# Performance work log

Measured on AMD Instinct MI355X. Metric: run time of the kernel, lower is better.

The kernel has to match this reference:

```python
import jax, jax.numpy as jnp
import numpy as np

DIM, NH, WS, SS, MLP_RATIO = 192, 6, 8, 4, 4
EPS = 1e-5


def _rel_pos_index(ws):
    coords = np.stack(np.meshgrid(np.arange(ws), np.arange(ws), indexing='ij')).reshape(2, -1)
    rel = (coords[:, :, None] - coords[:, None, :]).transpose(1, 2, 0)
    rel[:, :, 0] += ws - 1
    rel[:, :, 1] += ws - 1
    rel[:, :, 0] *= 2 * ws - 1
    return rel.sum(-1)  # (ws*ws, ws*ws) int


def _attn_mask(hp, wp, ws, ss):
    img = np.zeros((hp, wp))
    slices = (slice(0, -ws), slice(-ws, -ss), slice(-ss, None))
    cnt = 0
    for hs in slices:
        for vs in slices:
            img[hs, vs] = cnt
            cnt += 1
    mw = img.reshape(hp // ws, ws, wp // ws, ws).transpose(0, 2, 1, 3).reshape(-1, ws * ws)
    am = mw[:, None, :] - mw[:, :, None]  # (nW, N, N)
    return jnp.asarray(np.where(am != 0, -100.0, 0.0).astype(np.float32))


def _ln(x, g, b):
    mu = jnp.mean(x, axis=-1, keepdims=True)
    var = jnp.mean(jnp.square(x - mu), axis=-1, keepdims=True)
    return (x - mu) * jax.lax.rsqrt(var + EPS) * g + b


def setup_inputs():
    key = jax.random.key(0)
    ks = jax.random.split(key, 8)
    B, H, W, C = 8, 128, 128, DIM
    hid = C * MLP_RATIO
    n = lambda k, s: jax.random.normal(k, s, dtype=jnp.float32) * 0.02
    return {
        'x': jax.random.normal(ks[0], (B, H * W, C), dtype=jnp.float32),
        'h': H, 'w': W,
        'norm1_g': jnp.ones((C,), jnp.float32), 'norm1_b': jnp.zeros((C,), jnp.float32),
        'qkv_w': n(ks[1], (C, 3 * C)), 'qkv_b': jnp.zeros((3 * C,), jnp.float32),
        'proj_w': n(ks[2], (C, C)), 'proj_b': jnp.zeros((C,), jnp.float32),
        'rel_bias_table': n(ks[3], ((2 * WS - 1) ** 2, NH)),
        'norm2_g': jnp.ones((C,), jnp.float32), 'norm2_b': jnp.zeros((C,), jnp.float32),
        'fc1_w': n(ks[4], (C, hid)), 'fc1_b': jnp.zeros((hid,), jnp.float32),
        'fc2_w': n(ks[5], (hid, C)), 'fc2_b': jnp.zeros((C,), jnp.float32),
    }


def reference(x, h, w, norm1_g, norm1_b, qkv_w, qkv_b, proj_w, proj_b,
              rel_bias_table, norm2_g, norm2_b, fc1_w, fc1_b, fc2_w, fc2_b):
    B, L, C = x.shape
    ws, ss, nh = WS, SS, NH
    hd = C // nh
    scale = hd ** (-0.5)

    shortcut = x
    xg = _ln(x, norm1_g, norm1_b).reshape(B, h, w, C)

    pad_h = (-h) % ws
    pad_w = (-w) % ws
    if pad_h or pad_w:
        xg = jnp.pad(xg, ((0, 0), (0, pad_h), (0, pad_w), (0, 0)))
    hp, wp = h + pad_h, w + pad_w
    if ss > 0:
        xg = jnp.roll(xg, (-ss, -ss), axis=(1, 2))

    # window partition -> (nB, N, C)
    win = xg.reshape(B, hp // ws, ws, wp // ws, ws, C).transpose(0, 1, 3, 2, 4, 5).reshape(-1, ws * ws, C)
    nB, N, _ = win.shape

    qkv = (win @ qkv_w + qkv_b).reshape(nB, N, 3, nh, hd).transpose(2, 0, 3, 1, 4)
    q, k, v = qkv[0] * scale, qkv[1], qkv[2]  # (nB, nh, N, hd)

    attn = jnp.einsum('bhnd,bhmd->bhnm', q, k)  # (nB, nh, N, N)
    rpi = _rel_pos_index(ws)
    bias = rel_bias_table[rpi.reshape(-1)].reshape(N, N, nh).transpose(2, 0, 1)
    attn = attn + bias[None]
    if ss > 0:
        mask = _attn_mask(hp, wp, ws, ss)  # (nW, N, N)
        nW = mask.shape[0]
        attn = (attn.reshape(nB // nW, nW, nh, N, N) + mask[None, :, None]).reshape(nB, nh, N, N)
    attn = jax.nn.softmax(attn, axis=-1)

    out = jnp.einsum('bhnm,bhmd->bnhd', attn, v).reshape(nB, N, C)
    out = out @ proj_w + proj_b

    # window reverse
    out = out.reshape(B, hp // ws, wp // ws, ws, ws, C).transpose(0, 1, 3, 2, 4, 5).reshape(B, hp, wp, C)
    if ss > 0:
        out = jnp.roll(out, (ss, ss), axis=(1, 2))
    out = out[:, :h, :w].reshape(B, h * w, C)

    x = shortcut + out
    xn2 = _ln(x, norm2_g, norm2_b)
    mlp = jax.nn.gelu(xn2 @ fc1_w + fc1_b, approximate=False) @ fc2_w + fc2_b
    return x + mlp
```

## Files before the change

kernel.cpp:

```cpp
#include <hip/hip_runtime.h>

typedef unsigned short u16;
typedef unsigned int   u32;
typedef __attribute__((ext_vector_type(8))) short bf16x8;
typedef __attribute__((ext_vector_type(4))) float f32x4;

#define L_TOK   16384
#define C_DIM   192
#define HID_DIM 768

#define OFF_QKV  0
#define OFF_PROJ 110592
#define OFF_FC1  147456
#define OFF_FC2  294912
#define CVT_TOT  442368

union FragU { int4 i4; bf16x8 h8; };

#define MFMA_B16(a,b,c) __builtin_amdgcn_mfma_f32_16x16x32_bf16(a,b,c,0,0,0)

__device__ __forceinline__ u16 f2bf(float f) {
    u32 t; __builtin_memcpy(&t, &f, 4);
    t += 0x7FFFu + ((t >> 16) & 1u);
    return (u16)(t >> 16);
}

__global__ __launch_bounds__(256) void k_cvt(
    const float* __restrict__ qkvw, const float* __restrict__ projw,
    const float* __restrict__ fc1w, const float* __restrict__ fc2w,
    u16* __restrict__ ws)
{
    const int i = blockIdx.x * 256 + threadIdx.x;
    if (i >= CVT_TOT) return;
    float v; int dst;
    if (i < OFF_PROJ) {
        const int k = i / 576, col = i % 576;
        const int grp = col / 192, rem = col % 192;
        const int head = rem >> 5, dim = rem & 31;
        v = qkvw[i];
        dst = OFF_QKV + head * (96 * 192) + (grp * 32 + dim) * 192 + k;
    } else if (i < OFF_FC1) {
        const int s = i - OFF_PROJ;
        const int cin = s / 192, cout = s % 192;
        const int head = cin >> 5, j = cin & 31;
        v = projw[s];
        dst = OFF_PROJ + head * (192 * 32) + cout * 32 + j;
    } else if (i < OFF_FC2) {
        const int s = i - OFF_FC1;
        const int k = s / 768, h = s % 768;
        v = fc1w[s];
        dst = OFF_FC1 + h * 192 + k;
    } else {
        const int s = i - OFF_FC2;
        const int h = s / 192, c = s % 192;
        v = fc2w[s];
        dst = OFF_FC2 + c * 768 + h;
    }
    ws[dst] = f2bf(v);
}

__global__ __launch_bounds__(256, 2) void k_attnproj(
    const float* __restrict__ x, const float* __restrict__ g1v, const float* __restrict__ b1v,
    const u16* __restrict__ qkvwT, const float* __restrict__ qkvb,
    const float* __restrict__ relb, const u16* __restrict__ projT, const float* __restrict__ projb,
    float* __restrict__ x1)
{
    struct PW {
        u16 qsb[64 * 40];
        u16 ksb[64 * 40];
        u16 vsbT[32 * 72];
        u16 psb[64 * 72];
        u16 oh [64 * 40];
    };
    union SmemU {
        u16 xw[128 * 200];
        PW pw[2];
    };
    __shared__ __align__(16) SmemU u;
    __shared__ __align__(16) u16 wbuf[192 * 40];
    __shared__ float relbs[225 * 6];

    const int t  = threadIdx.x;
    const int lane = t & 63, w = t >> 6;
    const int win = w >> 1, half = w & 1;
    const int l15 = lane & 15, quad = lane >> 4;
    const int wi2 = blockIdx.x * 2 + win;
    const int b  = wi2 >> 8;
    const int hb = (wi2 >> 4) & 15;
    const int wb = wi2 & 15;
    const bool maskon = (hb == 15) || (wb == 15);
    const f32x4 zf = {0.f, 0.f, 0.f, 0.f};

    for (int i = t; i < 225 * 6; i += 256) relbs[i] = relb[i];

    #pragma unroll
    for (int tk = 0; tk < 2; ++tk) {
        const int nn = t >> 2, q4 = t & 3;
        const int tok = tk * 64 + nn;
        const int tw = tok >> 6, n = tok & 63;
        const int wiA = blockIdx.x * 2 + tw;
        const int bA  = wiA >> 8;
        const int hbA = (wiA >> 4) & 15, wbA = wiA & 15;
        const int r = n >> 3, c = n & 7;
        const int ho = (hbA * 8 + r + 4) & 127;
        const int wo = (wbA * 8 + c + 4) & 127;
        const size_t xoff = ((size_t)bA * L_TOK + ho * 128 + wo) * C_DIM;
        const float* xp = x + xoff + q4 * 48;
        float f[48];
        float sum = 0.f, sq = 0.f;
        #pragma unroll
        for (int i = 0; i < 12; ++i) {
            float4 v = *(const float4*)(xp + i * 4);
            f[i*4+0]=v.x; f[i*4+1]=v.y; f[i*4+2]=v.z; f[i*4+3]=v.w;
            sum += v.x+v.y+v.z+v.w;
            sq  += v.x*v.x + v.y*v.y + v.z*v.z + v.w*v.w;
        }
        sum += __shfl_xor(sum, 1); sum += __shfl_xor(sum, 2);
        sq  += __shfl_xor(sq, 1);  sq  += __shfl_xor(sq, 2);
        const float mu = sum * (1.f / 192.f);
        const float rstd = rsqrtf(sq * (1.f / 192.f) - mu * mu + 1e-5f);
        u16* xrow = u.xw + tok * 200 + q4 * 48;
        #pragma unroll
        for (int i = 0; i < 6; ++i) {
            u32 pk[4];
            #pragma unroll
            for (int j = 0; j < 4; ++j) {
                float g0 = g1v[q4*48 + i*8 + j*2],     b0 = b1v[q4*48 + i*8 + j*2];
                float g1 = g1v[q4*48 + i*8 + j*2 + 1], b1 = b1v[q4*48 + i*8 + j*2 + 1];
                float y0 = (f[i*8+j*2]   - mu) * rstd * g0 + b0;
                float y1 = (f[i*8+j*2+1] - mu) * rstd * g1 + b1;
                pk[j] = (u32)f2bf(y0) | (((u32)f2bf(y1)) << 16);
            }
            *(int4*)(xrow + i * 8) = make_int4((int)pk[0], (int)pk[1], (int)pk[2], (int)pk[3]);
        }
    }
    __syncthreads();

    FragU afrag[2][6];
    #pragma unroll
    for (int mt = 0; mt < 2; ++mt)
        #pragma unroll
        for (int kk = 0; kk < 6; ++kk)
            afrag[mt][kk].i4 = *(const int4*)(u.xw +
                (win*64 + half*32 + mt*16 + l15) * 200 + kk*32 + quad*8);

    PW* P = &u.pw[win];
    const int rb = half*32 + quad*4;

    int4 wr0, wr1, wr2;
    auto LOADW = [&](int hh, int sub) {
        if (sub < 3) {
            const u16* src = qkvwT + (size_t)hh * (96 * 192) + sub * 64;
            wr0 = *(const int4*)(src + ((t      ) >> 3) * 192 + ((t      ) & 7) * 8);
            wr1 = *(const int4*)(src + ((t + 256) >> 3) * 192 + ((t + 256) & 7) * 8);
            wr2 = *(const int4*)(src + ((t + 512) >> 3) * 192 + ((t + 512) & 7) * 8);
        } else {
            const u16* src = projT + (size_t)hh * (192 * 32);
            wr0 = *(const int4*)(src + ((t      ) >> 2) * 32 + ((t      ) & 3) * 8);
            wr1 = *(const int4*)(src + ((t + 256) >> 2) * 32 + ((t + 256) & 3) * 8);
            wr2 = *(const int4*)(src + ((t + 512) >> 2) * 32 + ((t + 512) & 3) * 8);
        }
    };
    auto STOREW = [&](int sub) {
        if (sub < 3) {
            *(int4*)(wbuf + ((t      ) >> 3) * 72 + ((t      ) & 7) * 8) = wr0;
            *(int4*)(wbuf + ((t + 256) >> 3) * 72 + ((t + 256) & 7) * 8) = wr1;
            *(int4*)(wbuf + ((t + 512) >> 3) * 72 + ((t + 512) & 7) * 8) = wr2;
        } else {
            *(int4*)(wbuf + ((t      ) >> 2) * 40 + ((t      ) & 3) * 8) = wr0;
            *(int4*)(wbuf + ((t + 256) >> 2) * 40 + ((t + 256) & 3) * 8) = wr1;
            *(int4*)(wbuf + ((t + 512) >> 2) * 40 + ((t + 512) & 3) * 8) = wr2;
        }
    };
    LOADW(0, 0);

    f32x4 acc2[2][12];
    #pragma unroll
    for (int mt = 0; mt < 2; ++mt)
        #pragma unroll
        for (int nt = 0; nt < 12; ++nt) acc2[mt][nt] = zf;

    for (int head = 0; head < 6; ++head) {
        f32x4 accq[2][6];
        #pragma unroll
        for (int mt = 0; mt < 2; ++mt)
            #pragma unroll
            for (int nt = 0; nt < 6; ++nt) accq[mt][nt] = zf;

        for (int kc = 0; kc < 3; ++kc) {
            __syncthreads();
            STOREW(kc);
            __syncthreads();
            LOADW(head, kc + 1);
            #pragma unroll
            for (int s = 0; s < 2; ++s) {
                #pragma unroll
                for (int nt = 0; nt < 6; ++nt) {
                    FragU bf_;
                    bf_.i4 = *(const int4*)(wbuf + (nt*16 + l15)*72 + s*32 + quad*8);
                    accq[0][nt] = MFMA_B16(afrag[0][kc*2 + s].h8, bf_.h8, accq[0][nt]);
                    accq[1][nt] = MFMA_B16(afrag[1][kc*2 + s].h8, bf_.h8, accq[1][nt]);
                }
            }
        }
        #pragma unroll
        for (int mt = 0; mt < 2; ++mt) {
            #pragma unroll
            for (int nt = 0; nt < 6; ++nt) {
                const int grp = nt >> 1;
                const int dim = (nt & 1)*16 + l15;
                const float bias = qkvb[grp*192 + head*32 + dim];
                float vv[4];
                #pragma unroll
                for (int rg = 0; rg < 4; ++rg) vv[rg] = accq[mt][nt][rg] + bias;
                const int rowb = rb + mt*16;
                if (grp == 0) {
                    #pragma unroll
                    for (int rg = 0; rg < 4; ++rg)
                        P->qsb[(rowb + rg)*40 + dim] = f2bf(vv[rg] * 0.17677669529663687f);
                } else if (grp == 1) {
                    #pragma unroll
                    for (int rg = 0; rg < 4; ++rg)
                        P->ksb[(rowb + rg)*40 + dim] = f2bf(vv[rg]);
                } else {
                    u32 lo = (u32)f2bf(vv[0]) | (((u32)f2bf(vv[1])) << 16);
                    u32 hi = (u32)f2bf(vv[2]) | (((u32)f2bf(vv[3])) << 16);
                    *(uint2*)&P->vsbT[dim*72 + rowb] = make_uint2(lo, hi);
                }
            }
        }
        __syncthreads();

        FragU qf0, qf1;
        qf0.i4 = *(const int4*)(P->qsb + (half*32 + l15)*40 + quad*8);
        qf1.i4 = *(const int4*)(P->qsb + (half*32 + 16 + l15)*40 + quad*8);
        f32x4 sv[2][4];
        #pragma unroll
        for (int nt = 0; nt < 4; ++nt) {
            FragU kf; kf.i4 = *(const int4*)(P->ksb + (nt*16 + l15)*40 + quad*8);
            sv[0][nt] = MFMA_B16(qf0.h8, kf.h8, zf);
            sv[1][nt] = MFMA_B16(qf1.h8, kf.h8, zf);
        }
        const int kr_ = l15 >> 3, kc2 = l15 & 7;
        #pragma unroll
        for (int mt = 0; mt < 2; ++mt) {
            #pragma unroll
            for (int rg = 0; rg < 4; ++rg) {
                const int qm = rb + mt*16 + rg;
                const int qr = qm >> 3, qc = qm & 7;
                #pragma unroll
                for (int nt = 0; nt < 4; ++nt) {
                    const int kr = nt*2 + kr_;
                    sv[mt][nt][rg] += relbs[((qr - kr + 7)*15 + (qc - kc2 + 7))*6 + head];
                }
            }
        }
        if (maskon) {
            #pragma unroll
            for (int mt = 0; mt < 2; ++mt) {
                #pragma unroll
                for (int rg = 0; rg < 4; ++rg) {
                    const int qm = rb + mt*16 + rg;
                    const int qr = qm >> 3, qc = qm & 7;
                    const int regq = ((hb == 15) ? (qr < 4 ? 1 : 2) : 0) * 3
                                   + ((wb == 15) ? (qc < 4 ? 1 : 2) : 0);
                    #pragma unroll
                    for (int nt = 0; nt < 4; ++nt) {
                        const int kr = nt*2 + kr_;
                        const int regk = ((hb == 15) ? (kr < 4 ? 1 : 2) : 0) * 3
                                       + ((wb == 15) ? (kc2 < 4 ? 1 : 2) : 0);
                        if (regq != regk) sv[mt][nt][rg] -= 100.f;
                    }
                }
            }
        }
        #pragma unroll
        for (int mt = 0; mt < 2; ++mt) {
            #pragma unroll
            for (int rg = 0; rg < 4; ++rg) {
                float mx = fmaxf(fmaxf(sv[mt][0][rg], sv[mt][1][rg]),
                                 fmaxf(sv[mt][2][rg], sv[mt][3][rg]));
                mx = fmaxf(mx, __shfl_xor(mx, 1));
                mx = fmaxf(mx, __shfl_xor(mx, 2));
                mx = fmaxf(mx, __shfl_xor(mx, 4));
                mx = fmaxf(mx, __shfl_xor(mx, 8));
                float s0 = 0.f;
                #pragma unroll
                for (int nt = 0; nt < 4; ++nt) {
                    sv[mt][nt][rg] = __expf(sv[mt][nt][rg] - mx); s0 += sv[mt][nt][rg];
                }
                s0 += __shfl_xor(s0, 1); s0 += __shfl_xor(s0, 2);
                s0 += __shfl_xor(s0, 4); s0 += __shfl_xor(s0, 8);
                const float inv = 1.f / s0;
                #pragma unroll
                for (int nt = 0; nt < 4; ++nt)
                    P->psb[(rb + mt*16 + rg)*72 + nt*16 + l15] = f2bf(sv[mt][nt][rg] * inv);
            }
        }

        FragU vb[2][2];
        #pragma unroll
        for (int ntv = 0; ntv < 2; ++ntv) {
            vb[ntv][0].i4 = *(const int4*)(P->vsbT + (ntv*16 + l15)*72 + quad*8);
            vb[ntv][1].i4 = *(const int4*)(P->vsbT + (ntv*16 + l15)*72 + 32 + quad*8);
        }
        #pragma unroll
        for (int mt = 0; mt < 2; ++mt) {
            FragU pa0, pa1;
            pa0.i4 = *(const int4*)(P->psb + (half*32 + mt*16 + l15)*72 + quad*8);
            pa1.i4 = *(const int4*)(P->psb + (half*32 + mt*16 + l15)*72 + 32 + quad*8);
            f32x4 ov0 = zf, ov1 = zf;
            ov0 = MFMA_B16(pa0.h8, vb[0][0].h8, ov0);
            ov0 = MFMA_B16(pa1.h8, vb[0][1].h8, ov0);
            ov1 = MFMA_B16(pa0.h8, vb[1][0].h8, ov1);
            ov1 = MFMA_B16(pa1.h8, vb[1][1].h8, ov1);
            #pragma unroll
            for (int rg = 0; rg < 4; ++rg) {
                P->oh[(rb + mt*16 + rg)*40 + l15]      = f2bf(ov0[rg]);
                P->oh[(rb + mt*16 + rg)*40 + 16 + l15] = f2bf(ov1[rg]);
            }
        }

        STOREW(3);
        __syncthreads();
        if (head < 5) LOADW(head + 1, 0);
        FragU ao0, ao1;
        ao0.i4 = *(const int4*)(P->oh + (half*32 + l15)*40 + quad*8);
        ao1.i4 = *(const int4*)(P->oh + (half*32 + 16 + l15)*40 + quad*8);
        #pragma unroll
        for (int nt = 0; nt < 12; ++nt) {
            FragU bp; bp.i4 = *(const int4*)(wbuf + (nt*16 + l15)*40 + quad*8);
            acc2[0][nt] = MFMA_B16(ao0.h8, bp.h8, acc2[0][nt]);
            acc2[1][nt] = MFMA_B16(ao1.h8, bp.h8, acc2[1][nt]);
        }
    }

    {
        float pb[12];
        #pragma unroll
        for (int nt = 0; nt < 12; ++nt) pb[nt] = projb[nt*16 + l15];
        #pragma unroll
        for (int mt = 0; mt < 2; ++mt) {
            #pragma unroll
            for (int rg = 0; rg < 4; ++rg) {
                const int tok = rb + mt*16 + rg;
                const int tr = tok >> 3, tc = tok & 7;
                const int ho2 = (hb * 8 + tr + 4) & 127;
                const int wo2 = (wb * 8 + tc + 4) & 127;
                const size_t base = ((size_t)b * L_TOK + ho2 * 128 + wo2) * C_DIM;
                #pragma unroll
                for (int nt = 0; nt < 12; ++nt) {
                    const int col = nt*16 + l15;
                    x1[base + col] = acc2[mt][nt][rg] + pb[nt] + x[base + col];
                }
            }
        }
    }
}

__global__ __launch_bounds__(256, 2) void k_mlp(
    const float* x1, const float* __restrict__ g2v, const float* __restrict__ b2v,
    const u16* __restrict__ fc1wT, const float* __restrict__ fc1b,
    const u16* __restrict__ fc2wT, const float* __restrict__ fc2b,
    float* out)
{
    union SmemU {
        u16 xnA[64 * 200];
        u16 hbuf[128 * 104];
    };
    __shared__ __align__(16) SmemU u;
    __shared__ __align__(16) u16 wT[2][7680];

    const int blk = blockIdx.x;
    const int t = threadIdx.x;
    const size_t row0 = (size_t)blk * 128;
    const int lane = t & 63, w = t >> 6;
    const int l15 = lane & 15, quad = lane >> 4;
    const f32x4 zf = {0.f, 0.f, 0.f, 0.f};

    FragU afrag[2][6];
    for (int hf = 0; hf < 2; ++hf) {
        const int nn = t >> 2, q4 = t & 3;
        const int tok = hf * 64 + nn;
        const float* xp = x1 + (row0 + tok) * C_DIM + q4 * 48;
        float f[48];
        float sum = 0.f, sq = 0.f;
        #pragma unroll
        for (int i = 0; i < 12; ++i) {
            float4 v = *(const float4*)(xp + i * 4);
            f[i*4+0]=v.x; f[i*4+1]=v.y; f[i*4+2]=v.z; f[i*4+3]=v.w;
            sum += v.x+v.y+v.z+v.w;
            sq  += v.x*v.x + v.y*v.y + v.z*v.z + v.w*v.w;
        }
        sum += __shfl_xor(sum,1); sum += __shfl_xor(sum,2);
        sq  += __shfl_xor(sq,1);  sq  += __shfl_xor(sq,2);
        const float mu = sum * (1.f/192.f);
        const float rstd = rsqrtf(sq * (1.f/192.f) - mu*mu + 1e-5f);
        u16* xrow = u.xnA + nn * 200 + q4 * 48;
        #pragma unroll
        for (int i = 0; i < 6; ++i) {
            u32 pk[4];
            #pragma unroll
            for (int j = 0; j < 4; ++j) {
                float g0 = g2v[q4*48 + i*8 + j*2],     b0 = b2v[q4*48 + i*8 + j*2];
                float g1 = g2v[q4*48 + i*8 + j*2 + 1], b1 = b2v[q4*48 + i*8 + j*2 + 1];
                float y0 = (f[i*8+j*2]   - mu) * rstd * g0 + b0;
                float y1 = (f[i*8+j*2+1] - mu) * rstd * g1 + b1;
                pk[j] = (u32)f2bf(y0) | (((u32)f2bf(y1)) << 16);
            }
            *(int4*)(xrow + i*8) = make_int4((int)pk[0], (int)pk[1], (int)pk[2], (int)pk[3]);
        }
        __syncthreads();
        #pragma unroll
        for (int kk = 0; kk < 6; ++kk)
            afrag[hf][kk].i4 = *(const int4*)(u.xnA + (w*16 + l15) * 200 + kk*32 + quad*8);
        __syncthreads();
    }

    int4 wr0, wr1, wr2;
    auto LOADW = [&](int hcL, int sub) {
        if (sub < 3) {
            const u16* src = fc1wT + (size_t)(hcL * 96) * 192 + sub * 64;
            wr0 = *(const int4*)(src + ((t      ) >> 3) * 192 + ((t      ) & 7) * 8);
            wr1 = *(const int4*)(src + ((t + 256) >> 3) * 192 + ((t + 256) & 7) * 8);
            wr2 = *(const int4*)(src + ((t + 512) >> 3) * 192 + ((t + 512) & 7) * 8);
        } else {
            const u16* src = fc2wT + hcL * 96 + (sub - 3) * 32;
            wr0 = *(const int4*)(src + ((t      ) >> 2) * 768 + ((t      ) & 3) * 8);
            wr1 = *(const int4*)(src + ((t + 256) >> 2) * 768 + ((t + 256) & 3) * 8);
            wr2 = *(const int4*)(src + ((t + 512) >> 2) * 768 + ((t + 512) & 3) * 8);
        }
    };
    auto STOREW = [&](u16* dstb, int sub) {
        if (sub < 3) {
            *(int4*)(dstb + ((t      ) >> 3) * 72 + ((t      ) & 7) * 8) = wr0;
            *(int4*)(dstb + ((t + 256) >> 3) * 72 + ((t + 256) & 7) * 8) = wr1;
            *(int4*)(dstb + ((t + 512) >> 3) * 72 + ((t + 512) & 7) * 8) = wr2;
        } else {
            *(int4*)(dstb + ((t      ) >> 2) * 40 + ((t      ) & 3) * 8) = wr0;
            *(int4*)(dstb + ((t + 256) >> 2) * 40 + ((t + 256) & 3) * 8) = wr1;
            *(int4*)(dstb + ((t + 512) >> 2) * 40 + ((t + 512) & 3) * 8) = wr2;
        }
    };
    LOADW(0, 0);

    f32x4 acc2[2][12];
    #pragma unroll
    for (int mt = 0; mt < 2; ++mt)
        #pragma unroll
        for (int nt = 0; nt < 12; ++nt) acc2[mt][nt] = zf;

    int g = 0;
    for (int hc = 0; hc < 8; ++hc) {
        f32x4 acc1[2][6];
        #pragma unroll
        for (int mt = 0; mt < 2; ++mt)
            #pragma unroll
            for (int nt = 0; nt < 6; ++nt) acc1[mt][nt] = zf;

        for (int kc = 0; kc < 3; ++kc) {
            u16* buf = wT[g & 1];
            STOREW(buf, kc);
            __syncthreads();
            LOADW(hc, kc + 1);
            #pragma unroll
            for (int s = 0; s < 2; ++s) {
                #pragma unroll
                for (int nt = 0; nt < 6; ++nt) {
                    FragU bf_;
                    bf_.i4 = *(const int4*)(buf + (nt*16 + l15)*72 + s*32 + quad*8);
                    acc1[0][nt] = MFMA_B16(afrag[0][kc*2 + s].h8, bf_.h8, acc1[0][nt]);
                    acc1[1][nt] = MFMA_B16(afrag[1][kc*2 + s].h8, bf_.h8, acc1[1][nt]);
                }
            }
            ++g;
        }
        #pragma unroll
        for (int nt = 0; nt < 6; ++nt) {
            const float bb = fc1b[hc*96 + nt*16 + l15];
            #pragma unroll
            for (int mt = 0; mt < 2; ++mt) {
                #pragma unroll
                for (int rg = 0; rg < 4; ++rg) {
                    float h = acc1[mt][nt][rg] + bb;
                    float e = __expf(h * (-1.5957691216057308f
                                          - 0.0713548162726302f * h * h));
                    float gl = h / (1.f + e);
                    u.hbuf[(mt*64 + w*16 + quad*4 + rg) * 104 + nt*16 + l15] = f2bf(gl);
                }
            }
        }
        for (int sc = 0; sc < 3; ++sc) {
            u16* buf = wT[g & 1];
            STOREW(buf, 3 + sc);
            __syncthreads();
            if (sc < 2)           LOADW(hc, 4 + sc);
            else if (hc < 7)      LOADW(hc + 1, 0);
            FragU ha0, ha1;
            ha0.i4 = *(const int4*)(u.hbuf + (w*16 + l15) * 104 + sc*32 + quad*8);
            ha1.i4 = *(const int4*)(u.hbuf + (64 + w*16 + l15) * 104 + sc*32 + quad*8);
            #pragma unroll
            for (int nt = 0; nt < 12; ++nt) {
                FragU bf_;
                bf_.i4 = *(const int4*)(buf + (nt*16 + l15)*40 + quad*8);
                acc2[0][nt] = MFMA_B16(ha0.h8, bf_.h8, acc2[0][nt]);
                acc2[1][nt] = MFMA_B16(ha1.h8, bf_.h8, acc2[1][nt]);
            }
            ++g;
        }
    }

    #pragma unroll
    for (int nt = 0; nt < 12; ++nt) {
        const int col = nt*16 + l15;
        const float bb = fc2b[col];
        #pragma unroll
        for (int mt = 0; mt < 2; ++mt) {
            #pragma unroll
            for (int rg = 0; rg < 4; ++rg) {
                const size_t idx = (row0 + mt*64 + w*16 + quad*4 + rg) * C_DIM + col;
                out[idx] = acc2[mt][nt][rg] + bb + x1[idx];
            }
        }
    }
}

extern "C" void kernel_launch(void* const* d_in, const int* in_sizes, int n_in,
                              void* d_out, int out_size, void* d_ws, size_t ws_size,
                              hipStream_t stream) {
    const float* x     = (const float*)d_in[0];
    const float* g1v   = (const float*)d_in[3];
    const float* b1v   = (const float*)d_in[4];
    const float* qkvw  = (const float*)d_in[5];
    const float* qkvb  = (const float*)d_in[6];
    const float* projw = (const float*)d_in[7];
    const float* projb = (const float*)d_in[8];
    const float* relb  = (const float*)d_in[9];
    const float* g2v   = (const float*)d_in[10];
    const float* b2v   = (const float*)d_in[11];
    const float* fc1w  = (const float*)d_in[12];
    const float* fc1b  = (const float*)d_in[13];
    const float* fc2w  = (const float*)d_in[14];
    const float* fc2b  = (const float*)d_in[15];

    float* x1 = (float*)d_out;
    u16* wsb  = (u16*)d_ws;

    hipLaunchKernelGGL(k_cvt, dim3((CVT_TOT + 255) / 256), dim3(256), 0, stream,
                       qkvw, projw, fc1w, fc2w, wsb);
    hipLaunchKernelGGL(k_attnproj, dim3(1024), dim3(256), 0, stream,
                       x, g1v, b1v, wsb + OFF_QKV, qkvb, relb, wsb + OFF_PROJ, projb, x1);
    hipLaunchKernelGGL(k_mlp, dim3(1024), dim3(256), 0, stream,
                       x1, g2v, b2v, wsb + OFF_FC1, fc1b, wsb + OFF_FC2, fc2b, x1);
}
```

Measured before the change: 524.3 us.

## Pre-tile MLP weights with XOR swizzle and stream them via direct global-to-LDS loads

The conversion kernel now writes fc1 and fc2 bf16 weights as contiguous per-stage 6144-element tiles, with an XOR swizzle on the inner index. The MLP kernel then fetches each stage with asynchronous global_load_lds instructions straight into a double-buffered shared tile. This replaces the register-staged global load and LDS store round trip, and swaps padded LDS rows for the swizzle to avoid bank conflicts. The aim is to cut register pressure and VALU/LDS-store work in the weight pipeline. It relies on __syncthreads waiting for the outstanding direct-to-LDS loads before the tile is read.

Measured after the change: 513.6 us. 1.02x faster.

```diff
diff --git a/kernel.cpp b/kernel.cpp
--- a/kernel.cpp
+++ b/kernel.cpp
@@ -49,12 +49,18 @@
         const int s = i - OFF_FC1;
         const int k = s / 768, h = s % 768;
         v = fc1w[s];
-        dst = OFF_FC1 + h * 192 + k;
+        const int hc = h / 96, cc = h % 96;
+        const int kc = k >> 6, ko = k & 63;
+        const int q = cc * 64 + (ko ^ ((cc & 7) << 3));
+        dst = OFF_FC1 + (hc * 3 + kc) * 6144 + q;
     } else {
         const int s = i - OFF_FC2;
         const int h = s / 192, c = s % 192;
         v = fc2w[s];
-        dst = OFF_FC2 + c * 768 + h;
+        const int hc = h / 96, rem = h % 96;
+        const int sc = rem >> 5, ho = rem & 31;
+        const int q = c * 32 + (ho ^ ((c & 3) << 3));
+        dst = OFF_FC2 + (hc * 3 + sc) * 6144 + q;
     }
     ws[dst] = f2bf(v);
 }
@@ -369,7 +375,7 @@
         u16 hbuf[128 * 104];
     };
     __shared__ __align__(16) SmemU u;
-    __shared__ __align__(16) u16 wT[2][7680];
+    __shared__ __align__(16) u16 wbig[2][6144];
 
     const int blk = blockIdx.x;
     const int t = threadIdx.x;
@@ -377,6 +383,22 @@
     const int lane = t & 63, w = t >> 6;
     const int l15 = lane & 15, quad = lane >> 4;
     const f32x4 zf = {0.f, 0.f, 0.f, 0.f};
+
+    auto issue_stage = [&](int st) {
+        const int hcs = st / 6, sub = st % 6;
+        const u16* src = (sub < 3) ? fc1wT + (hcs * 3 + sub) * 6144
+                                   : fc2wT + (hcs * 3 + (sub - 3)) * 6144;
+        u16* dstb = &wbig[st & 1][0];
+        #pragma unroll
+        for (int c = 0; c < 3; ++c) {
+            const int cid = c * 4 + w;
+            __builtin_amdgcn_global_load_lds(
+                (const __attribute__((address_space(1))) void*)(src + cid * 512 + lane * 8),
+                (__attribute__((address_space(3))) void*)(dstb + cid * 512),
+                16, 0, 0);
+        }
+    };
+    issue_stage(0);
 
     FragU afrag[2][6];
     for (int hf = 0; hf < 2; ++hf) {
@@ -417,33 +439,6 @@
         __syncthreads();
     }
 
-    int4 wr0, wr1, wr2;
-    auto LOADW = [&](int hcL, int sub) {
-        if (sub < 3) {
-            const u16* src = fc1wT + (size_t)(hcL * 96) * 192 + sub * 64;
-            wr0 = *(const int4*)(src + ((t      ) >> 3) * 192 + ((t      ) & 7) * 8);
-            wr1 = *(const int4*)(src + ((t + 256) >> 3) * 192 + ((t + 256) & 7) * 8);
-            wr2 = *(const int4*)(src + ((t + 512) >> 3) * 192 + ((t + 512) & 7) * 8);
-        } else {
-            const u16* src = fc2wT + hcL * 96 + (sub - 3) * 32;
-            wr0 = *(const int4*)(src + ((t      ) >> 2) * 768 + ((t      ) & 3) * 8);
-            wr1 = *(const int4*)(src + ((t + 256) >> 2) * 768 + ((t + 256) & 3) * 8);
-            wr2 = *(const int4*)(src + ((t + 512) >> 2) * 768 + ((t + 512) & 3) * 8);
-        }
-    };
-    auto STOREW = [&](u16* dstb, int sub) {
-        if (sub < 3) {
-            *(int4*)(dstb + ((t      ) >> 3) * 72 + ((t      ) & 7) * 8) = wr0;
-            *(int4*)(dstb + ((t + 256) >> 3) * 72 + ((t + 256) & 7) * 8) = wr1;
-            *(int4*)(dstb + ((t + 512) >> 3) * 72 + ((t + 512) & 7) * 8) = wr2;
-        } else {
-            *(int4*)(dstb + ((t      ) >> 2) * 40 + ((t      ) & 3) * 8) = wr0;
-            *(int4*)(dstb + ((t + 256) >> 2) * 40 + ((t + 256) & 3) * 8) = wr1;
-            *(int4*)(dstb + ((t + 512) >> 2) * 40 + ((t + 512) & 3) * 8) = wr2;
-        }
-    };
-    LOADW(0, 0);
-
     f32x4 acc2[2][12];
     #pragma unroll
     for (int mt = 0; mt < 2; ++mt)
@@ -459,16 +454,17 @@
             for (int nt = 0; nt < 6; ++nt) acc1[mt][nt] = zf;
 
         for (int kc = 0; kc < 3; ++kc) {
-            u16* buf = wT[g & 1];
-            STOREW(buf, kc);
             __syncthreads();
-            LOADW(hc, kc + 1);
+            if (g < 47) issue_stage(g + 1);
+            const u16* buf = &wbig[g & 1][0];
             #pragma unroll
             for (int s = 0; s < 2; ++s) {
                 #pragma unroll
                 for (int nt = 0; nt < 6; ++nt) {
+                    const int row = nt*16 + l15;
                     FragU bf_;
-                    bf_.i4 = *(const int4*)(buf + (nt*16 + l15)*72 + s*32 + quad*8);
+                    bf_.i4 = *(const int4*)(buf + row*64 +
+                                            ((s*32 + quad*8) ^ ((row & 7) << 3)));
                     acc1[0][nt] = MFMA_B16(afrag[0][kc*2 + s].h8, bf_.h8, acc1[0][nt]);
                     acc1[1][nt] = MFMA_B16(afrag[1][kc*2 + s].h8, bf_.h8, acc1[1][nt]);
                 }
@@ -491,18 +487,18 @@
             }
         }
         for (int sc = 0; sc < 3; ++sc) {
-            u16* buf = wT[g & 1];
-            STOREW(buf, 3 + sc);
             __syncthreads();
-            if (sc < 2)           LOADW(hc, 4 + sc);
-            else if (hc < 7)      LOADW(hc + 1, 0);
+            if (g < 47) issue_stage(g + 1);
+            const u16* buf = &wbig[g & 1][0];
             FragU ha0, ha1;
             ha0.i4 = *(const int4*)(u.hbuf + (w*16 + l15) * 104 + sc*32 + quad*8);
             ha1.i4 = *(const int4*)(u.hbuf + (64 + w*16 + l15) * 104 + sc*32 + quad*8);
             #pragma unroll
             for (int nt = 0; nt < 12; ++nt) {
+                const int row = nt*16 + l15;
                 FragU bf_;
-                bf_.i4 = *(const int4*)(buf + (nt*16 + l15)*40 + quad*8);
+                bf_.i4 = *(const int4*)(buf + row*32 +
+                                        ((quad*8) ^ ((row & 3) << 3)));
                 acc2[0][nt] = MFMA_B16(ha0.h8, bf_.h8, acc2[0][nt]);
                 acc2[1][nt] = MFMA_B16(ha1.h8, bf_.h8, acc2[1][nt]);
             }
```
